# Optimization experiments

Hardware: AMD Instinct MI355X
Metric: run time of the kernel (lower is better)

The kernel has to match this reference:

```python
import jax, jax.numpy as jnp
import numpy as np
import math

D_MODEL = 1024
N_HEADS = 16
Q_PROJ = D_MODEL // 4
KV_PROJ = D_MODEL // 4
DH = D_MODEL // N_HEADS
LN_EPS = 1e-5


def _layernorm(x, gamma, beta):
    mu = jnp.mean(x, axis=-1, keepdims=True)
    var = jnp.mean(jnp.square(x - mu), axis=-1, keepdims=True)
    return (x - mu) * jax.lax.rsqrt(var + LN_EPS) * gamma + beta


def setup_inputs() -> dict:
    key = jax.random.key(0)
    ks = jax.random.split(key, 7)
    B, S = 2, 2048
    x = jax.random.normal(ks[0], (B, S, D_MODEL), dtype=jnp.float32)
    W_dq = 0.01 * jax.random.normal(ks[1], (D_MODEL, Q_PROJ), dtype=jnp.float32)
    W_uq = 0.01 * jax.random.normal(ks[2], (Q_PROJ, D_MODEL), dtype=jnp.float32)
    W_dkv = 0.01 * jax.random.normal(ks[3], (D_MODEL, KV_PROJ), dtype=jnp.float32)
    W_ukv = 0.01 * jax.random.normal(ks[4], (KV_PROJ, 2 * D_MODEL), dtype=jnp.float32)
    W_o = 0.01 * jax.random.normal(ks[5], (D_MODEL, D_MODEL), dtype=jnp.float32)
    return {
        "x": x,
        "W_dq": W_dq, "W_uq": W_uq,
        "q_ln_g": jnp.ones((Q_PROJ,), jnp.float32), "q_ln_b": jnp.zeros((Q_PROJ,), jnp.float32),
        "W_dkv": W_dkv, "W_ukv": W_ukv,
        "kv_ln_g": jnp.ones((KV_PROJ,), jnp.float32), "kv_ln_b": jnp.zeros((KV_PROJ,), jnp.float32),
        "W_o": W_o,
    }


def reference(x, W_dq, W_uq, q_ln_g, q_ln_b, W_dkv, W_ukv, kv_ln_g, kv_ln_b, W_o):
    B, S, D = x.shape
    # low-rank Q path
    cq = _layernorm(x @ W_dq, q_ln_g, q_ln_b)          # [B,S,q_proj]
    Q = cq @ W_uq                                       # [B,S,D]
    # low-rank KV path
    ckv = _layernorm(x @ W_dkv, kv_ln_g, kv_ln_b)       # [B,S,kv_proj]
    KV = ckv @ W_ukv                                    # [B,S,2D]
    K, V = KV[..., :D], KV[..., D:]
    q = Q.reshape(B, S, N_HEADS, DH)
    k = K.reshape(B, S, N_HEADS, DH)
    v = V.reshape(B, S, N_HEADS, DH)
    scores = jnp.einsum("bqhd,bkhd->bhqk", q, k) / math.sqrt(float(DH))
    # faithful to original: multiply by tril mask, then set exact zeros to -inf
    mask = jnp.tril(jnp.ones((S, S), dtype=scores.dtype))
    scores = scores * mask
    scores = jnp.where(scores == 0, -jnp.inf, scores)
    attn = jax.nn.softmax(scores, axis=-1)
    out = jnp.einsum("bhqk,bkhd->bqhd", attn, v).reshape(B, S, D)
    return out @ W_o.T
```

## Files before the change

### kernel.cpp

```cpp
#include <hip/hip_runtime.h>

typedef __bf16 bf16;
typedef __bf16 bf16x4 __attribute__((ext_vector_type(4)));
typedef __bf16 bf16x8 __attribute__((ext_vector_type(8)));
typedef float f32x4 __attribute__((ext_vector_type(4)));

#define D_MODEL 1024
#define PROJ    256
#define SEQ     2048
#define BATCH   2
#define TOK     4096
#define NH      16
#define DH      64
#define NEG_BIG (-1e30f)
#define QSCALE  0.18033688011112042f

#if __has_builtin(__builtin_amdgcn_exp2f)
#define EXP2(x) __builtin_amdgcn_exp2f(x)
#else
#define EXP2(x) exp2f(x)
#endif

typedef __attribute__((address_space(3))) unsigned int  lds_u32;
typedef __attribute__((address_space(1))) unsigned int  glb_u32;

__device__ __forceinline__ void gl2lds16(const void* gsrc, void* ldst) {
    __builtin_amdgcn_global_load_lds((const glb_u32*)gsrc, (lds_u32*)ldst, 16, 0, 0);
}

template <int CTRL>
__device__ __forceinline__ float dppmov(float x) {
    int i = __builtin_bit_cast(int, x);
    i = __builtin_amdgcn_update_dpp(i, i, CTRL, 0xf, 0xf, false);
    return __builtin_bit_cast(float, i);
}
__device__ __forceinline__ float rowsum16(float v) {
    v += dppmov<0xB1>(v);
    v += dppmov<0x4E>(v);
    v += dppmov<0x141>(v);
    v += dppmov<0x140>(v);
    return v;
}

__global__ __launch_bounds__(256) void prep_kernel(
    const float* __restrict__ W_o, const float* __restrict__ x,
    const float* __restrict__ W_dq, const float* __restrict__ W_dkv,
    const float* __restrict__ W_uq, const float* __restrict__ W_ukv,
    bf16* __restrict__ Wo16, bf16* __restrict__ x16,
    bf16* __restrict__ Wt_dq, bf16* __restrict__ Wt_dkv,
    bf16* __restrict__ Wt_uq, bf16* __restrict__ Wt_ukv) {
    if (blockIdx.x < 320) {
        __shared__ float tile[64][65];
        int t = blockIdx.x;
        const float* src; bf16* dst; int R, C;
        if (t < 64)       { src = W_dq;  dst = Wt_dq;  R = 1024; C = 256; }
        else if (t < 128) { src = W_dkv; dst = Wt_dkv; R = 1024; C = 256;  t -= 64; }
        else if (t < 192) { src = W_uq;  dst = Wt_uq;  R = 256;  C = 1024; t -= 128; }
        else              { src = W_ukv; dst = Wt_ukv; R = 256;  C = 2048; t -= 192; }
        const int tilesC = C >> 6;
        const int r0 = (t / tilesC) << 6;
        const int c0 = (t % tilesC) << 6;
        const int tr = threadIdx.x >> 6;
        const int tc = threadIdx.x & 63;
#pragma unroll
        for (int i = 0; i < 16; ++i)
            tile[tr * 16 + i][tc] = src[(size_t)(r0 + tr * 16 + i) * C + c0 + tc];
        __syncthreads();
#pragma unroll
        for (int i = 0; i < 16; ++i)
            dst[(size_t)(c0 + tr * 16 + i) * R + r0 + tc] =
                (bf16)tile[tc][tr * 16 + i];
    } else {
        const int NW = 262144;
        const int NX = 1048576;
        for (int i = (blockIdx.x - 320) * 256 + threadIdx.x; i < NW + NX;
             i += 1024 * 256) {
            if (i < NW) {
                float4 v = ((const float4*)W_o)[i];
                bf16x4 p;
                p[0] = (bf16)v.x; p[1] = (bf16)v.y;
                p[2] = (bf16)v.z; p[3] = (bf16)v.w;
                ((bf16x4*)Wo16)[i] = p;
            } else {
                int j = i - NW;
                float4 v = ((const float4*)x)[j];
                bf16x4 p;
                p[0] = (bf16)v.x; p[1] = (bf16)v.y;
                p[2] = (bf16)v.z; p[3] = (bf16)v.w;
                ((bf16x4*)x16)[j] = p;
            }
        }
    }
}

__global__ __launch_bounds__(256) void gemm_ln_kernel(
    const bf16* __restrict__ x16,
    const bf16* __restrict__ Wt_q, const bf16* __restrict__ Wt_kv,
    const float* __restrict__ q_g, const float* __restrict__ q_b,
    const float* __restrict__ kv_g, const float* __restrict__ kv_b,
    bf16* __restrict__ cq, bf16* __restrict__ ckv) {
    __shared__ alignas(16) bf16 xA[2][16 * 32];
    __shared__ alignas(16) bf16 wB[2][256 * 32];
    __shared__ float red1[4][16];
    __shared__ float red2[4][16];

    const int K = 1024;
    const bf16* Wt = blockIdx.y ? Wt_kv : Wt_q;
    const float* gamma = blockIdx.y ? kv_g : q_g;
    const float* beta  = blockIdx.y ? kv_b : q_b;
    bf16* out = blockIdx.y ? ckv : cq;

    const int m0 = blockIdx.x * 16;
    const int wv = threadIdx.x >> 6;
    const int lane = threadIdx.x & 63;
    const int g = lane >> 4;
    const int ln16 = lane & 15;

    const int crow = lane >> 2;
    const int ckc = lane & 3;
    const bf16* gx = x16 + (size_t)(m0 + crow) * K + ckc * 8;
    const bf16* gw = Wt + (size_t)(64 * wv + crow) * K + ckc * 8;

    f32x4 acc[4] = {};

    if (wv == 0) gl2lds16(gx, (char*)xA);
#pragma unroll
    for (int i = 0; i < 4; ++i)
        gl2lds16(gw + (size_t)i * 16 * K, (char*)wB + wv * 4096 + i * 1024);
    __syncthreads();

    int buf = 0;
    for (int k0 = 0; k0 < K; k0 += 32) {
        if (k0 + 32 < K) {
            const int nb = buf ^ 1;
            if (wv == 0) gl2lds16(gx + k0 + 32, (char*)xA + nb * 1024);
#pragma unroll
            for (int i = 0; i < 4; ++i)
                gl2lds16(gw + (size_t)i * 16 * K + k0 + 32,
                         (char*)wB + nb * 16384 + wv * 4096 + i * 1024);
        }
        const bf16* cx = &xA[buf][0];
        const bf16* cw = &wB[buf][0];
        bf16x8 a = *(const bf16x8*)(cx + ln16 * 32 + g * 8);
#pragma unroll
        for (int t = 0; t < 4; ++t) {
            bf16x8 b = *(const bf16x8*)(cw + (wv * 64 + 16 * t + ln16) * 32 + g * 8);
            acc[t] = __builtin_amdgcn_mfma_f32_16x16x32_bf16(a, b, acc[t], 0, 0, 0);
        }
        __syncthreads();
        buf ^= 1;
    }

    float s1[4], s2[4];
#pragma unroll
    for (int r = 0; r < 4; ++r) {
        float a = 0.f, b = 0.f;
#pragma unroll
        for (int t = 0; t < 4; ++t) { float v = acc[t][r]; a += v; b += v * v; }
        s1[r] = rowsum16(a); s2[r] = rowsum16(b);
    }
    if (ln16 == 0) {
#pragma unroll
        for (int r = 0; r < 4; ++r) {
            red1[wv][g * 4 + r] = s1[r];
            red2[wv][g * 4 + r] = s2[r];
        }
    }
    __syncthreads();
#pragma unroll
    for (int r = 0; r < 4; ++r) {
        int rl = g * 4 + r;
        float t1 = red1[0][rl] + red1[1][rl] + red1[2][rl] + red1[3][rl];
        float t2 = red2[0][rl] + red2[1][rl] + red2[2][rl] + red2[3][rl];
        float mu = t1 * (1.0f / 256.0f);
        float var = t2 * (1.0f / 256.0f) - mu * mu;
        float rs = rsqrtf(var + 1e-5f);
        int row = m0 + rl;
#pragma unroll
        for (int t = 0; t < 4; ++t) {
            int col = wv * 64 + 16 * t + ln16;
            float v = (acc[t][r] - mu) * rs * gamma[col] + beta[col];
            out[(size_t)row * PROJ + col] = (bf16)v;
        }
    }
}

__device__ __forceinline__ void gemm_body128(
    const bf16* __restrict__ A, const bf16* __restrict__ Bt,
    bf16* __restrict__ C, bf16* __restrict__ C2, int K,
    int bx, int by, int mode, bf16* tA, bf16* tB) {
    const int w = threadIdx.x >> 6;
    const int lane = threadIdx.x & 63;
    const int g = lane >> 4;
    const int ln16 = lane & 15;
    const int wr = w >> 1;
    const int wc = w & 1;

    const int m0 = bx * 128;
    const int n0 = by * 128;

    const int crow = lane >> 2;
    const int ckc = lane & 3;
    const bf16* gA0 = A  + (size_t)(m0 + 32 * w + crow) * K + ckc * 8;
    const bf16* gA1 = gA0 + (size_t)16 * K;
    const bf16* gB0 = Bt + (size_t)(n0 + 32 * w + crow) * K + ckc * 8;
    const bf16* gB1 = gB0 + (size_t)16 * K;

    f32x4 acc[4][4] = {};

    gl2lds16(gA0, (char*)tA + w * 2048);
    gl2lds16(gA1, (char*)tA + w * 2048 + 1024);
    gl2lds16(gB0, (char*)tB + w * 2048);
    gl2lds16(gB1, (char*)tB + w * 2048 + 1024);
    __syncthreads();

    int buf = 0;
    for (int k0 = 0; k0 < K; k0 += 32) {
        if (k0 + 32 < K) {
            const int nb = buf ^ 1;
            gl2lds16(gA0 + k0 + 32, (char*)tA + nb * 8192 + w * 2048);
            gl2lds16(gA1 + k0 + 32, (char*)tA + nb * 8192 + w * 2048 + 1024);
            gl2lds16(gB0 + k0 + 32, (char*)tB + nb * 8192 + w * 2048);
            gl2lds16(gB1 + k0 + 32, (char*)tB + nb * 8192 + w * 2048 + 1024);
        }
        const bf16* cA = tA + buf * 4096;
        const bf16* cB = tB + buf * 4096;

        bf16x8 af[4], bfr[4];
#pragma unroll
        for (int s = 0; s < 4; ++s)
            af[s] = *(const bf16x8*)(cA + (wr * 64 + s * 16 + ln16) * 32 + g * 8);
#pragma unroll
        for (int t = 0; t < 4; ++t)
            bfr[t] = *(const bf16x8*)(cB + (wc * 64 + t * 16 + ln16) * 32 + g * 8);
        __builtin_amdgcn_s_setprio(1);
#pragma unroll
        for (int s = 0; s < 4; ++s)
#pragma unroll
            for (int t = 0; t < 4; ++t)
                acc[s][t] = __builtin_amdgcn_mfma_f32_16x16x32_bf16(
                    af[s], bfr[t], acc[s][t], 0, 0, 0);
        __builtin_amdgcn_s_setprio(0);
        __syncthreads();
        buf ^= 1;
    }

#pragma unroll
    for (int s = 0; s < 4; ++s)
#pragma unroll
        for (int t = 0; t < 4; ++t) {
            const int col = n0 + wc * 64 + t * 16 + ln16;
            const int tok0 = m0 + wr * 64 + s * 16 + g * 4;
            if (mode == 2 && col >= 1024) {
                int cc = col - 1024;
                int h = cc >> 6, d = cc & 63;
                int b = tok0 >> 11, sq = tok0 & 2047;
                bf16x4 pk;
#pragma unroll
                for (int r = 0; r < 4; ++r) pk[r] = (bf16)acc[s][t][r];
                *(bf16x4*)(C2 + ((size_t)((b * 16 + h) * 64 + d) * SEQ + sq)) = pk;
            } else {
#pragma unroll
                for (int r = 0; r < 4; ++r) {
                    int row = tok0 + r;
                    float v = acc[s][t][r];
                    if (mode == 1) v *= QSCALE;
                    int h = col >> 6, d = col & 63;
                    int b = row >> 11, sq = row & 2047;
                    C[((size_t)((b * 16 + h) * 2048 + sq)) * 64 + d] = (bf16)v;
                }
            }
        }
}

__global__ __launch_bounds__(256) void gemm_qkv_kernel(
    const bf16* __restrict__ cq, const bf16* __restrict__ Wt_uq,
    const bf16* __restrict__ ckv, const bf16* __restrict__ Wt_ukv,
    bf16* __restrict__ Qh, bf16* __restrict__ Kh, bf16* __restrict__ Vt) {
    __shared__ alignas(16) bf16 tA[2][128 * 32];
    __shared__ alignas(16) bf16 tB[2][128 * 32];
    const int i = blockIdx.x;
    if (i < 256) {
        gemm_body128(cq, Wt_uq, Qh, nullptr, PROJ,
                     i >> 3, i & 7, 1, &tA[0][0], &tB[0][0]);
    } else {
        const int j = i - 256;
        gemm_body128(ckv, Wt_ukv, Kh, Vt, PROJ,
                     j >> 4, j & 15, 2, &tA[0][0], &tB[0][0]);
    }
}

__device__ __forceinline__ void gemm_body(
    const bf16* __restrict__ A, const bf16* __restrict__ Bt,
    float* __restrict__ C, int N, int K,
    int bx, int by, bf16* tA, bf16* tB) {
    const int w = threadIdx.x >> 6;
    const int lane = threadIdx.x & 63;
    const int g = lane >> 4;
    const int ln16 = lane & 15;
    const int wr = w >> 1;
    const int wc = w & 1;

    const int m0 = bx * 64;
    const int n0 = by * 128;

    const int crow = lane >> 2;
    const int ckc = lane & 3;
    const bf16* gA  = A  + (size_t)(m0 + w * 16 + crow) * K + ckc * 8;
    const bf16* gB0 = Bt + (size_t)(n0 + w * 16 + crow) * K + ckc * 8;
    const bf16* gB1 = Bt + (size_t)(n0 + 64 + w * 16 + crow) * K + ckc * 8;

    f32x4 acc[2][4] = {};

    gl2lds16(gA, (char*)tA + w * 1024);
    gl2lds16(gB0, (char*)tB + w * 1024);
    gl2lds16(gB1, (char*)tB + 4096 + w * 1024);
    __syncthreads();

    int buf = 0;
    for (int k0 = 0; k0 < K; k0 += 32) {
        if (k0 + 32 < K) {
            const int nb = buf ^ 1;
            gl2lds16(gA + k0 + 32, (char*)tA + nb * 4096 + w * 1024);
            gl2lds16(gB0 + k0 + 32, (char*)tB + nb * 8192 + w * 1024);
            gl2lds16(gB1 + k0 + 32, (char*)tB + nb * 8192 + 4096 + w * 1024);
        }
        const bf16* cA = tA + buf * 2048;
        const bf16* cB = tB + buf * 4096;

        bf16x8 af[2], bfr[4];
#pragma unroll
        for (int s = 0; s < 2; ++s)
            af[s] = *(const bf16x8*)(cA + (wr * 32 + s * 16 + ln16) * 32 + g * 8);
#pragma unroll
        for (int t = 0; t < 4; ++t)
            bfr[t] = *(const bf16x8*)(cB + (wc * 64 + t * 16 + ln16) * 32 + g * 8);
        __builtin_amdgcn_s_setprio(1);
#pragma unroll
        for (int s = 0; s < 2; ++s)
#pragma unroll
            for (int t = 0; t < 4; ++t)
                acc[s][t] = __builtin_amdgcn_mfma_f32_16x16x32_bf16(
                    af[s], bfr[t], acc[s][t], 0, 0, 0);
        __builtin_amdgcn_s_setprio(0);
        __syncthreads();
        buf ^= 1;
    }

#pragma unroll
    for (int s = 0; s < 2; ++s)
#pragma unroll
        for (int t = 0; t < 4; ++t) {
            const int col = n0 + wc * 64 + t * 16 + ln16;
            const int tok0 = m0 + wr * 32 + s * 16 + g * 4;
#pragma unroll
            for (int r = 0; r < 4; ++r)
                C[(size_t)(tok0 + r) * N + col] = acc[s][t][r];
        }
}

__global__ __launch_bounds__(256) void gemm_o_kernel(
    const bf16* __restrict__ A, const bf16* __restrict__ Bt,
    float* __restrict__ C, int M, int N, int K) {
    __shared__ alignas(16) bf16 tA[2][64 * 32];
    __shared__ alignas(16) bf16 tB[2][128 * 32];
    gemm_body(A, Bt, C, N, K, blockIdx.x, blockIdx.y, &tA[0][0], &tB[0][0]);
}

__device__ __forceinline__ void qk_exp_pack(
    int k0, int q, bool masked, int g, int ln16,
    bf16x8 aq0, bf16x8 aq1, const bf16x8* Kf,
    bf16x8& P1, bf16x8& P2) {
    f32x4 sc[4];
    __builtin_amdgcn_s_setprio(1);
#pragma unroll
    for (int c = 0; c < 4; ++c) {
        f32x4 z = {};
        z = __builtin_amdgcn_mfma_f32_16x16x32_bf16(Kf[2 * c], aq0, z, 0, 0, 0);
        z = __builtin_amdgcn_mfma_f32_16x16x32_bf16(Kf[2 * c + 1], aq1, z, 0, 0, 0);
        sc[c] = z;
    }
    __builtin_amdgcn_s_setprio(0);
    if (masked) {
        const int kb = k0 + 8 * g;
#pragma unroll
        for (int c = 0; c < 4; ++c)
#pragma unroll
            for (int r = 0; r < 4; ++r) {
                int kcol = kb + (c & 1) * 4 + r + ((c >> 1) << 5);
                if (kcol > q) sc[c][r] = NEG_BIG;
            }
    }
#pragma unroll
    for (int c = 0; c < 4; ++c)
#pragma unroll
        for (int r = 0; r < 4; ++r) sc[c][r] = EXP2(sc[c][r]);
#pragma unroll
    for (int r = 0; r < 4; ++r) {
        P1[r] = (bf16)sc[0][r]; P1[4 + r] = (bf16)sc[1][r];
        P2[r] = (bf16)sc[2][r]; P2[4 + r] = (bf16)sc[3][r];
    }
}

__device__ __forceinline__ void pv_accum(
    bf16x8 P1, bf16x8 P2, const bf16x8* Vf, bf16x8 vones,
    f32x4* o, f32x4& oli) {
    __builtin_amdgcn_s_setprio(1);
#pragma unroll
    for (int t = 0; t < 4; ++t) {
        o[t] = __builtin_amdgcn_mfma_f32_16x16x32_bf16(Vf[2 * t], P1, o[t], 0, 0, 0);
        o[t] = __builtin_amdgcn_mfma_f32_16x16x32_bf16(Vf[2 * t + 1], P2, o[t], 0, 0, 0);
    }
    oli = __builtin_amdgcn_mfma_f32_16x16x32_bf16(vones, P1, oli, 0, 0, 0);
    oli = __builtin_amdgcn_mfma_f32_16x16x32_bf16(vones, P2, oli, 0, 0, 0);
    __builtin_amdgcn_s_setprio(0);
}

__global__ __launch_bounds__(128) void attn_kernel(
    const bf16* __restrict__ Qh, const bf16* __restrict__ Kh,
    const bf16* __restrict__ Vt, bf16* __restrict__ AT) {
    __shared__ alignas(128) bf16 kbuf[2][64 * 64];
    __shared__ alignas(128) bf16 vbuf[2][64 * 64];

    const int lane = threadIdx.x & 63;
    const int g = lane >> 4;
    const int ln16 = lane & 15;
    const int wv = threadIdx.x >> 6;

    const int bh = blockIdx.x & 31;
    const int qsuper = 31 - (blockIdx.x >> 5);
    const int nt = qsuper + 1;
    const int qb = qsuper * 64 + wv * 32;

    const bf16* Kbh = Kh + (size_t)bh * SEQ * DH;
    const bf16* Vbh = Vt + (size_t)bh * DH * SEQ;

    const int rho = lane >> 3;
    const int sl  = lane & 7;
    int kofs[4];
    size_t vofs[4];
#pragma unroll
    for (int i = 0; i < 4; ++i) {
        const int row = 32 * wv + 8 * i + rho;
        const int c = sl ^ ((rho & 3) | ((i & 1) << 2));
        kofs[i] = row * 64 + c * 8;
        vofs[i] = (size_t)row * SEQ + c * 8;
    }

    const int row_base = ((ln16 & 12) << 1) + (ln16 & 3);
    int kro[4], vro[4];
#pragma unroll
    for (int c = 0; c < 4; ++c) {
        const int row = row_base + (c & 1) * 4 + ((c >> 1) << 5);
        const int fr = (row & 3) | (((row >> 3) & 1) << 2);
        kro[c] = row * 128 + (g ^ fr) * 16;
    }
#pragma unroll
    for (int t = 0; t < 4; ++t) {
        const int d = 16 * t + ln16;
        const int fd = (d & 3) | (((d >> 3) & 1) << 2);
        vro[t] = d * 128 + (g ^ fd) * 16;
    }

    bf16x8 aq[2][2];
#pragma unroll
    for (int hh = 0; hh < 2; ++hh) {
        const bf16* qp = Qh + ((size_t)bh * SEQ + qb + 16 * hh + ln16) * DH + g * 8;
        aq[hh][0] = *(const bf16x8*)qp;
        aq[hh][1] = *(const bf16x8*)(qp + 32);
    }

    bf16x8 vones;
#pragma unroll
    for (int i = 0; i < 8; ++i) vones[i] = (bf16)1.0f;

    f32x4 o0[4] = {}, o1[4] = {};
    f32x4 oli0 = {}, oli1 = {};

#pragma unroll
    for (int i = 0; i < 4; ++i) {
        gl2lds16(Kbh + kofs[i], (char*)kbuf + wv * 4096 + i * 1024);
        gl2lds16(Vbh + vofs[i], (char*)vbuf + wv * 4096 + i * 1024);
    }
    __syncthreads();

    int cur = 0;
    for (int kt = 0; kt < nt; ++kt) {
        if (kt + 1 < nt) {
            const size_t k0n = (size_t)(kt + 1) * 64;
            char* kb = (char*)kbuf + (cur ^ 1) * 8192 + wv * 4096;
            char* vb = (char*)vbuf + (cur ^ 1) * 8192 + wv * 4096;
#pragma unroll
            for (int i = 0; i < 4; ++i) {
                gl2lds16(Kbh + k0n * 64 + kofs[i], kb + i * 1024);
                gl2lds16(Vbh + vofs[i] + k0n, vb + i * 1024);
            }
        }

        const char* kb = (const char*)kbuf + cur * 8192;
        const char* vb = (const char*)vbuf + cur * 8192;
        bf16x8 Kf[8], Vf[8];
#pragma unroll
        for (int c = 0; c < 4; ++c) {
            Kf[2 * c]     = *(const bf16x8*)(kb + kro[c]);
            Kf[2 * c + 1] = *(const bf16x8*)(kb + (kro[c] ^ 64));
        }
#pragma unroll
        for (int t = 0; t < 4; ++t) {
            Vf[2 * t]     = *(const bf16x8*)(vb + vro[t]);
            Vf[2 * t + 1] = *(const bf16x8*)(vb + (vro[t] ^ 64));
        }

        const int k0 = kt * 64;
        const bool msk = (kt == qsuper);
        bf16x8 P1a, P2a, P1b, P2b;
        qk_exp_pack(k0, qb + ln16, msk, g, ln16,
                    aq[0][0], aq[0][1], Kf, P1a, P2a);
        qk_exp_pack(k0, qb + 16 + ln16, msk, g, ln16,
                    aq[1][0], aq[1][1], Kf, P1b, P2b);
        pv_accum(P1a, P2a, Vf, vones, o0, oli0);
        pv_accum(P1b, P2b, Vf, vones, o1, oli1);
        __syncthreads();
        cur ^= 1;
    }

    const float inv0 = 1.0f / oli0[0];
    const float inv1 = 1.0f / oli1[0];
    const int b = bh >> 4, h = bh & 15;
    const size_t tok0 = (size_t)(b * SEQ + qb + ln16) * D_MODEL + h * DH;
    const size_t tok1 = (size_t)(b * SEQ + qb + 16 + ln16) * D_MODEL + h * DH;
#pragma unroll
    for (int t = 0; t < 4; ++t) {
        bf16x4 pk0, pk1;
#pragma unroll
        for (int r = 0; r < 4; ++r) {
            pk0[r] = (bf16)(o0[t][r] * inv0);
            pk1[r] = (bf16)(o1[t][r] * inv1);
        }
        *(bf16x4*)(AT + tok0 + 16 * t + 4 * g) = pk0;
        *(bf16x4*)(AT + tok1 + 16 * t + 4 * g) = pk1;
    }
}

extern "C" void kernel_launch(void* const* d_in, const int* in_sizes, int n_in,
                              void* d_out, int out_size, void* d_ws, size_t ws_size,
                              hipStream_t stream) {
    const float* x     = (const float*)d_in[0];
    const float* W_dq  = (const float*)d_in[1];
    const float* W_uq  = (const float*)d_in[2];
    const float* q_g   = (const float*)d_in[3];
    const float* q_b   = (const float*)d_in[4];
    const float* W_dkv = (const float*)d_in[5];
    const float* W_ukv = (const float*)d_in[6];
    const float* kv_g  = (const float*)d_in[7];
    const float* kv_b  = (const float*)d_in[8];
    const float* W_o   = (const float*)d_in[9];

    char* ws = (char*)d_ws;
    size_t off = 0;
    bf16* Wo16   = (bf16*)(ws + off); off += (size_t)D_MODEL * D_MODEL * 2;
    bf16* Wt_dq  = (bf16*)(ws + off); off += (size_t)PROJ * D_MODEL * 2;
    bf16* Wt_dkv = (bf16*)(ws + off); off += (size_t)PROJ * D_MODEL * 2;
    bf16* Wt_uq  = (bf16*)(ws + off); off += (size_t)D_MODEL * PROJ * 2;
    bf16* Wt_ukv = (bf16*)(ws + off); off += (size_t)(2 * D_MODEL) * PROJ * 2;
    bf16* x16    = (bf16*)(ws + off); off += (size_t)TOK * D_MODEL * 2;
    bf16* cq     = (bf16*)(ws + off); off += (size_t)TOK * PROJ * 2;
    bf16* ckv    = (bf16*)(ws + off); off += (size_t)TOK * PROJ * 2;
    bf16* Qh     = (bf16*)(ws + off); off += (size_t)TOK * D_MODEL * 2;
    bf16* Kh     = (bf16*)(ws + off); off += (size_t)TOK * D_MODEL * 2;
    bf16* Vt     = (bf16*)(ws + off); off += (size_t)TOK * D_MODEL * 2;
    bf16* AT     = (bf16*)(ws + off); off += (size_t)TOK * D_MODEL * 2;

    prep_kernel<<<1344, 256, 0, stream>>>(
        W_o, x, W_dq, W_dkv, W_uq, W_ukv,
        Wo16, x16, Wt_dq, Wt_dkv, Wt_uq, Wt_ukv);

    gemm_ln_kernel<<<dim3(TOK / 16, 2), 256, 0, stream>>>(
        x16, Wt_dq, Wt_dkv, q_g, q_b, kv_g, kv_b, cq, ckv);

    gemm_qkv_kernel<<<768, 256, 0, stream>>>(cq, Wt_uq, ckv, Wt_ukv, Qh, Kh, Vt);

    attn_kernel<<<1024, 128, 0, stream>>>(Qh, Kh, Vt, AT);

    gemm_o_kernel<<<dim3(TOK / 64, D_MODEL / 128), 256, 0, stream>>>(
        AT, Wo16, (float*)d_out, TOK, D_MODEL, D_MODEL);
}
```

Baseline: 187.9 us.

## Prefetch two stages ahead with explicit vmcnt waits in GEMM and attention loops

Replaces the double-buffered loops in the projection, QKV, output GEMMs and the attention kernel with a schedule that prefetches stage s+2. Each stage reads fragments into registers, waits for LDS reads to finish, then issues global-to-LDS loads into the just-consumed buffer before the MFMAs. Partial vmcnt waits let the next stage's loads stay in flight across the barrier instead of draining with __syncthreads each iteration. It adds a second barrier per stage and depends on the hand-written vmcnt counts matching the number of outstanding loads.

```diff
diff --git a/kernel.cpp b/kernel.cpp
--- a/kernel.cpp
+++ b/kernel.cpp
@@ -27,6 +27,11 @@
 __device__ __forceinline__ void gl2lds16(const void* gsrc, void* ldst) {
     __builtin_amdgcn_global_load_lds((const glb_u32*)gsrc, (lds_u32*)ldst, 16, 0, 0);
 }
+
+#define VM_WAIT(N) asm volatile("s_waitcnt vmcnt(" #N ")" ::: "memory")
+#define LGKM0      asm volatile("s_waitcnt lgkmcnt(0)" ::: "memory")
+#define SCHEDB()   __builtin_amdgcn_sched_barrier(0)
+#define SBAR()     __builtin_amdgcn_s_barrier()
 
 template <int CTRL>
 __device__ __forceinline__ float dppmov(float x) {
@@ -122,33 +127,44 @@
     const bf16* gw = Wt + (size_t)(64 * wv + crow) * K + ckc * 8;
 
     f32x4 acc[4] = {};
-
-    if (wv == 0) gl2lds16(gx, (char*)xA);
-#pragma unroll
-    for (int i = 0; i < 4; ++i)
-        gl2lds16(gw + (size_t)i * 16 * K, (char*)wB + wv * 4096 + i * 1024);
-    __syncthreads();
-
-    int buf = 0;
-    for (int k0 = 0; k0 < K; k0 += 32) {
-        if (k0 + 32 < K) {
-            const int nb = buf ^ 1;
-            if (wv == 0) gl2lds16(gx + k0 + 32, (char*)xA + nb * 1024);
+    const int nst = K >> 5;
+
+#pragma unroll
+    for (int s = 0; s < 2; ++s) {
+        gl2lds16(gx + s * 32, (char*)xA + s * 1024);
+#pragma unroll
+        for (int i = 0; i < 4; ++i)
+            gl2lds16(gw + (size_t)i * 16 * K + s * 32,
+                     (char*)wB + s * 16384 + wv * 4096 + i * 1024);
+    }
+    VM_WAIT(0); SCHEDB(); SBAR();
+
+    for (int s = 0; s < nst; ++s) {
+        if (s > 0) {
+            if (s + 1 < nst) { VM_WAIT(5); } else { VM_WAIT(0); }
+            SCHEDB(); SBAR();
+        }
+        const bf16* cx = (const bf16*)((const char*)xA + (s & 1) * 1024);
+        const bf16* cw = (const bf16*)((const char*)wB + (s & 1) * 16384);
+        bf16x8 a = *(const bf16x8*)(cx + ln16 * 32 + g * 8);
+        bf16x8 bb[4];
+#pragma unroll
+        for (int t = 0; t < 4; ++t)
+            bb[t] = *(const bf16x8*)(cw + (wv * 64 + 16 * t + ln16) * 32 + g * 8);
+        LGKM0; SCHEDB(); SBAR();
+        if (s + 2 < nst) {
+            const int k2 = (s + 2) * 32;
+            gl2lds16(gx + k2, (char*)xA + (s & 1) * 1024);
 #pragma unroll
             for (int i = 0; i < 4; ++i)
-                gl2lds16(gw + (size_t)i * 16 * K + k0 + 32,
-                         (char*)wB + nb * 16384 + wv * 4096 + i * 1024);
-        }
-        const bf16* cx = &xA[buf][0];
-        const bf16* cw = &wB[buf][0];
-        bf16x8 a = *(const bf16x8*)(cx + ln16 * 32 + g * 8);
-#pragma unroll
-        for (int t = 0; t < 4; ++t) {
-            bf16x8 b = *(const bf16x8*)(cw + (wv * 64 + 16 * t + ln16) * 32 + g * 8);
-            acc[t] = __builtin_amdgcn_mfma_f32_16x16x32_bf16(a, b, acc[t], 0, 0, 0);
-        }
-        __syncthreads();
-        buf ^= 1;
+                gl2lds16(gw + (size_t)i * 16 * K + k2,
+                         (char*)wB + (s & 1) * 16384 + wv * 4096 + i * 1024);
+        }
+        __builtin_amdgcn_s_setprio(1);
+#pragma unroll
+        for (int t = 0; t < 4; ++t)
+            acc[t] = __builtin_amdgcn_mfma_f32_16x16x32_bf16(a, bb[t], acc[t], 0, 0, 0);
+        __builtin_amdgcn_s_setprio(0);
     }
 
     float s1[4], s2[4];
@@ -207,63 +223,69 @@
     const bf16* gB1 = gB0 + (size_t)16 * K;
 
     f32x4 acc[4][4] = {};
-
-    gl2lds16(gA0, (char*)tA + w * 2048);
-    gl2lds16(gA1, (char*)tA + w * 2048 + 1024);
-    gl2lds16(gB0, (char*)tB + w * 2048);
-    gl2lds16(gB1, (char*)tB + w * 2048 + 1024);
-    __syncthreads();
-
-    int buf = 0;
-    for (int k0 = 0; k0 < K; k0 += 32) {
-        if (k0 + 32 < K) {
-            const int nb = buf ^ 1;
-            gl2lds16(gA0 + k0 + 32, (char*)tA + nb * 8192 + w * 2048);
-            gl2lds16(gA1 + k0 + 32, (char*)tA + nb * 8192 + w * 2048 + 1024);
-            gl2lds16(gB0 + k0 + 32, (char*)tB + nb * 8192 + w * 2048);
-            gl2lds16(gB1 + k0 + 32, (char*)tB + nb * 8192 + w * 2048 + 1024);
-        }
-        const bf16* cA = tA + buf * 4096;
-        const bf16* cB = tB + buf * 4096;
+    const int nst = K >> 5;
+
+#pragma unroll
+    for (int s = 0; s < 2; ++s) {
+        gl2lds16(gA0 + s * 32, (char*)tA + s * 8192 + w * 2048);
+        gl2lds16(gA1 + s * 32, (char*)tA + s * 8192 + w * 2048 + 1024);
+        gl2lds16(gB0 + s * 32, (char*)tB + s * 8192 + w * 2048);
+        gl2lds16(gB1 + s * 32, (char*)tB + s * 8192 + w * 2048 + 1024);
+    }
+    VM_WAIT(0); SCHEDB(); SBAR();
+
+    for (int s = 0; s < nst; ++s) {
+        if (s > 0) {
+            if (s + 1 < nst) { VM_WAIT(4); } else { VM_WAIT(0); }
+            SCHEDB(); SBAR();
+        }
+        const bf16* cA = tA + (s & 1) * 4096;
+        const bf16* cB = tB + (s & 1) * 4096;
 
         bf16x8 af[4], bfr[4];
 #pragma unroll
-        for (int s = 0; s < 4; ++s)
-            af[s] = *(const bf16x8*)(cA + (wr * 64 + s * 16 + ln16) * 32 + g * 8);
+        for (int q = 0; q < 4; ++q)
+            af[q] = *(const bf16x8*)(cA + (wr * 64 + q * 16 + ln16) * 32 + g * 8);
 #pragma unroll
         for (int t = 0; t < 4; ++t)
             bfr[t] = *(const bf16x8*)(cB + (wc * 64 + t * 16 + ln16) * 32 + g * 8);
+        LGKM0; SCHEDB(); SBAR();
+        if (s + 2 < nst) {
+            const int k2 = (s + 2) * 32;
+            gl2lds16(gA0 + k2, (char*)tA + (s & 1) * 8192 + w * 2048);
+            gl2lds16(gA1 + k2, (char*)tA + (s & 1) * 8192 + w * 2048 + 1024);
+            gl2lds16(gB0 + k2, (char*)tB + (s & 1) * 8192 + w * 2048);
+            gl2lds16(gB1 + k2, (char*)tB + (s & 1) * 8192 + w * 2048 + 1024);
+        }
         __builtin_amdgcn_s_setprio(1);
 #pragma unroll
-        for (int s = 0; s < 4; ++s)
+        for (int q = 0; q < 4; ++q)
 #pragma unroll
             for (int t = 0; t < 4; ++t)
-                acc[s][t] = __builtin_amdgcn_mfma_f32_16x16x32_bf16(
-                    af[s], bfr[t], acc[s][t], 0, 0, 0);
+                acc[q][t] = __builtin_amdgcn_mfma_f32_16x16x32_bf16(
+                    af[q], bfr[t], acc[q][t], 0, 0, 0);
         __builtin_amdgcn_s_setprio(0);
-        __syncthreads();
-        buf ^= 1;
-    }
-
-#pragma unroll
-    for (int s = 0; s < 4; ++s)
+    }
+
+#pragma unroll
+    for (int q = 0; q < 4; ++q)
 #pragma unroll
         for (int t = 0; t < 4; ++t) {
             const int col = n0 + wc * 64 + t * 16 + ln16;
-            const int tok0 = m0 + wr * 64 + s * 16 + g * 4;
+            const int tok0 = m0 + wr * 64 + q * 16 + g * 4;
             if (mode == 2 && col >= 1024) {
                 int cc = col - 1024;
                 int h = cc >> 6, d = cc & 63;
                 int b = tok0 >> 11, sq = tok0 & 2047;
                 bf16x4 pk;
 #pragma unroll
-                for (int r = 0; r < 4; ++r) pk[r] = (bf16)acc[s][t][r];
+                for (int r = 0; r < 4; ++r) pk[r] = (bf16)acc[q][t][r];
                 *(bf16x4*)(C2 + ((size_t)((b * 16 + h) * 64 + d) * SEQ + sq)) = pk;
             } else {
 #pragma unroll
                 for (int r = 0; r < 4; ++r) {
                     int row = tok0 + r;
-                    float v = acc[s][t][r];
+                    float v = acc[q][t][r];
                     if (mode == 1) v *= QSCALE;
                     int h = col >> 6, d = col & 63;
                     int b = row >> 11, sq = row & 2047;
@@ -311,51 +333,57 @@
     const bf16* gB1 = Bt + (size_t)(n0 + 64 + w * 16 + crow) * K + ckc * 8;
 
     f32x4 acc[2][4] = {};
-
-    gl2lds16(gA, (char*)tA + w * 1024);
-    gl2lds16(gB0, (char*)tB + w * 1024);
-    gl2lds16(gB1, (char*)tB + 4096 + w * 1024);
-    __syncthreads();
-
-    int buf = 0;
-    for (int k0 = 0; k0 < K; k0 += 32) {
-        if (k0 + 32 < K) {
-            const int nb = buf ^ 1;
-            gl2lds16(gA + k0 + 32, (char*)tA + nb * 4096 + w * 1024);
-            gl2lds16(gB0 + k0 + 32, (char*)tB + nb * 8192 + w * 1024);
-            gl2lds16(gB1 + k0 + 32, (char*)tB + nb * 8192 + 4096 + w * 1024);
-        }
-        const bf16* cA = tA + buf * 2048;
-        const bf16* cB = tB + buf * 4096;
+    const int nst = K >> 5;
+
+#pragma unroll
+    for (int s = 0; s < 2; ++s) {
+        gl2lds16(gA + s * 32, (char*)tA + s * 4096 + w * 1024);
+        gl2lds16(gB0 + s * 32, (char*)tB + s * 8192 + w * 1024);
+        gl2lds16(gB1 + s * 32, (char*)tB + s * 8192 + 4096 + w * 1024);
+    }
+    VM_WAIT(0); SCHEDB(); SBAR();
+
+    for (int s = 0; s < nst; ++s) {
+        if (s > 0) {
+            if (s + 1 < nst) { VM_WAIT(3); } else { VM_WAIT(0); }
+            SCHEDB(); SBAR();
+        }
+        const bf16* cA = tA + (s & 1) * 2048;
+        const bf16* cB = tB + (s & 1) * 4096;
 
         bf16x8 af[2], bfr[4];
 #pragma unroll
-        for (int s = 0; s < 2; ++s)
-            af[s] = *(const bf16x8*)(cA + (wr * 32 + s * 16 + ln16) * 32 + g * 8);
+        for (int q = 0; q < 2; ++q)
+            af[q] = *(const bf16x8*)(cA + (wr * 32 + q * 16 + ln16) * 32 + g * 8);
 #pragma unroll
         for (int t = 0; t < 4; ++t)
             bfr[t] = *(const bf16x8*)(cB + (wc * 64 + t * 16 + ln16) * 32 + g * 8);
+        LGKM0; SCHEDB(); SBAR();
+        if (s + 2 < nst) {
+            const int k2 = (s + 2) * 32;
+            gl2lds16(gA + k2, (char*)tA + (s & 1) * 4096 + w * 1024);
+            gl2lds16(gB0 + k2, (char*)tB + (s & 1) * 8192 + w * 1024);
+            gl2lds16(gB1 + k2, (char*)tB + (s & 1) * 8192 + 4096 + w * 1024);
+        }
         __builtin_amdgcn_s_setprio(1);
 #pragma unroll
-        for (int s = 0; s < 2; ++s)
+        for (int q = 0; q < 2; ++q)
 #pragma unroll
             for (int t = 0; t < 4; ++t)
-                acc[s][t] = __builtin_amdgcn_mfma_f32_16x16x32_bf16(
-                    af[s], bfr[t], acc[s][t], 0, 0, 0);
+                acc[q][t] = __builtin_amdgcn_mfma_f32_16x16x32_bf16(
+                    af[q], bfr[t], acc[q][t], 0, 0, 0);
         __builtin_amdgcn_s_setprio(0);
-        __syncthreads();
-        buf ^= 1;
-    }
-
-#pragma unroll
-    for (int s = 0; s < 2; ++s)
+    }
+
+#pragma unroll
+    for (int q = 0; q < 2; ++q)
 #pragma unroll
         for (int t = 0; t < 4; ++t) {
             const int col = n0 + wc * 64 + t * 16 + ln16;
-            const int tok0 = m0 + wr * 32 + s * 16 + g * 4;
+            const int tok0 = m0 + wr * 32 + q * 16 + g * 4;
 #pragma unroll
             for (int r = 0; r < 4; ++r)
-                C[(size_t)(tok0 + r) * N + col] = acc[s][t][r];
+                C[(size_t)(tok0 + r) * N + col] = acc[q][t][r];
         }
 }
 
@@ -482,23 +510,24 @@
         gl2lds16(Kbh + kofs[i], (char*)kbuf + wv * 4096 + i * 1024);
         gl2lds16(Vbh + vofs[i], (char*)vbuf + wv * 4096 + i * 1024);
     }
-    __syncthreads();
-
-    int cur = 0;
+    if (nt > 1) {
+#pragma unroll
+        for (int i = 0; i < 4; ++i) {
+            gl2lds16(Kbh + (size_t)64 * 64 + kofs[i],
+                     (char*)kbuf + 8192 + wv * 4096 + i * 1024);
+            gl2lds16(Vbh + vofs[i] + 64,
+                     (char*)vbuf + 8192 + wv * 4096 + i * 1024);
+        }
+    }
+    VM_WAIT(0); SCHEDB(); SBAR();
+
     for (int kt = 0; kt < nt; ++kt) {
-        if (kt + 1 < nt) {
-            const size_t k0n = (size_t)(kt + 1) * 64;
-            char* kb = (char*)kbuf + (cur ^ 1) * 8192 + wv * 4096;
-            char* vb = (char*)vbuf + (cur ^ 1) * 8192 + wv * 4096;
-#pragma unroll
-            for (int i = 0; i < 4; ++i) {
-                gl2lds16(Kbh + k0n * 64 + kofs[i], kb + i * 1024);
-                gl2lds16(Vbh + vofs[i] + k0n, vb + i * 1024);
-            }
-        }
-
-        const char* kb = (const char*)kbuf + cur * 8192;
-        const char* vb = (const char*)vbuf + cur * 8192;
+        if (kt > 0) {
+            if (kt + 1 < nt) { VM_WAIT(8); } else { VM_WAIT(0); }
+            SCHEDB(); SBAR();
+        }
+        const char* kb = (const char*)kbuf + (kt & 1) * 8192;
+        const char* vb = (const char*)vbuf + (kt & 1) * 8192;
         bf16x8 Kf[8], Vf[8];
 #pragma unroll
         for (int c = 0; c < 4; ++c) {
@@ -509,6 +538,17 @@
         for (int t = 0; t < 4; ++t) {
             Vf[2 * t]     = *(const bf16x8*)(vb + vro[t]);
             Vf[2 * t + 1] = *(const bf16x8*)(vb + (vro[t] ^ 64));
+        }
+        LGKM0; SCHEDB(); SBAR();
+        if (kt + 2 < nt) {
+            const size_t k0n = (size_t)(kt + 2) * 64;
+            char* kd = (char*)kbuf + (kt & 1) * 8192 + wv * 4096;
+            char* vd = (char*)vbuf + (kt & 1) * 8192 + wv * 4096;
+#pragma unroll
+            for (int i = 0; i < 4; ++i) {
+                gl2lds16(Kbh + k0n * 64 + kofs[i], kd + i * 1024);
+                gl2lds16(Vbh + vofs[i] + k0n, vd + i * 1024);
+            }
         }
 
         const int k0 = kt * 64;
@@ -520,8 +560,6 @@
                     aq[1][0], aq[1][1], Kf, P1b, P2b);
         pv_accum(P1a, P2a, Vf, vones, o0, oli0);
         pv_accum(P1b, P2b, Vf, vones, o1, oli1);
-        __syncthreads();
-        cur ^= 1;
     }
 
     const float inv0 = 1.0f / oli0[0];
```

After: 180.2 us. -4.1%, faster.
